# Kernel tuning notes

Measured on AMD Instinct MI355X. Metric: run time of the kernel, lower is better.

## Reference

```python
import jax, jax.numpy as jnp
import numpy as np

B, S, HID, H = 1, 2048, 2048, 16
D = HID // H
EPS = 1e-6


def _rotate_half(x):
    x1, x2 = jnp.split(x, 2, axis=-1)
    return jnp.concatenate([-x2, x1], axis=-1)


def _apply_rope(q, k, cos, sin):
    # cos, sin: [S, D] -> broadcast over [B, H, S, D]
    c = cos[None, None, :, :]
    s = sin[None, None, :, :]
    return q * c + _rotate_half(q) * s, k * c + _rotate_half(k) * s


def _proj_heads(x, W):
    # x: [B,S,HID], W: [HID_out, HID_in] (torch Linear convention) -> [B,H,S,D]
    y = jnp.einsum('bsh,oh->bso', x, W)
    return y.reshape(B, S, H, D).transpose(0, 2, 1, 3)


def setup_inputs() -> dict:
    key = jax.random.key(0)
    ks = jax.random.split(key, 12)
    inp = {
        'hidden_states_mu': jax.random.normal(ks[0], (B, S, HID), jnp.float32),
        'hidden_states_log_sigma': jax.random.normal(ks[1], (B, S, HID), jnp.float32) * 0.1,
    }
    # proper rotary tables
    inv_freq = 1.0 / (10000.0 ** (np.arange(0, D, 2, dtype=np.float32) / D))
    pos = np.arange(S, dtype=np.float32)
    freqs = np.outer(pos, inv_freq)                      # [S, D/2]
    emb = np.concatenate([freqs, freqs], axis=-1)        # [S, D]
    inp['cos'] = jnp.asarray(np.cos(emb), jnp.float32)
    inp['sin'] = jnp.asarray(np.sin(emb), jnp.float32)
    names = ['Wq_mu', 'Wk_mu', 'Wv_mu', 'Wo_mu', 'Wq_sigma', 'Wk_sigma', 'Wv_sigma', 'Wo_sigma']
    for i, n in enumerate(names):
        inp[n] = jax.random.normal(ks[2 + i], (HID, HID), jnp.float32) * 0.02
    inp['tau'] = jnp.ones((1,), jnp.float32)
    return inp


def reference(hidden_states_mu, hidden_states_log_sigma, cos, sin,
              Wq_mu, Wk_mu, Wv_mu, Wo_mu,
              Wq_sigma, Wk_sigma, Wv_sigma, Wo_sigma, tau):
    q_mu = _proj_heads(hidden_states_mu, Wq_mu)
    k_mu = _proj_heads(hidden_states_mu, Wk_mu)
    v_mu = _proj_heads(hidden_states_mu, Wv_mu)
    q_ls = _proj_heads(hidden_states_log_sigma, Wq_sigma)
    k_ls = _proj_heads(hidden_states_log_sigma, Wk_sigma)
    v_ls = _proj_heads(hidden_states_log_sigma, Wv_sigma)

    q_mu, k_mu = _apply_rope(q_mu, k_mu, cos, sin)

    # squared W2 distance between means
    dot_mu = jnp.einsum('bhqd,bhkd->bhqk', q_mu, k_mu)
    dist_mu_sq = (jnp.sum(q_mu ** 2, -1)[..., :, None]
                  + jnp.sum(k_mu ** 2, -1)[..., None, :]
                  - 2.0 * dot_mu)

    # squared W2 distance between sigmas
    sig_q = jnp.exp(0.5 * q_ls)
    sig_k = jnp.exp(0.5 * k_ls)
    dot_s = jnp.einsum('bhqd,bhkd->bhqk', sig_q, sig_k)
    dist_sigma_sq = (jnp.sum(sig_q ** 2, -1)[..., :, None]
                     + jnp.sum(sig_k ** 2, -1)[..., None, :]
                     - 2.0 * dot_s)

    denom = jnp.abs(tau[0]) + EPS
    attn = jax.nn.softmax(-(dist_mu_sq + dist_sigma_sq) / denom, axis=-1)

    out_mu = jnp.einsum('bhqk,bhkd->bhqd', attn, v_mu)
    out_ls = jnp.einsum('bhqk,bhkd->bhqd', attn, v_ls)
    out_mu = out_mu.transpose(0, 2, 1, 3).reshape(B, S, HID)
    out_ls = out_ls.transpose(0, 2, 1, 3).reshape(B, S, HID)
    out_mu = jnp.einsum('bsh,oh->bso', out_mu, Wo_mu)
    out_ls = jnp.einsum('bsh,oh->bso', out_ls, Wo_sigma)
    return out_mu, out_ls
```

## Files before the change

kernel.cpp:

```cpp
#include <hip/hip_runtime.h>
#include <hip/hip_bf16.h>

#define S_LEN 2048
#define HIDDEN 2048
#define NH 16
#define HD 128

typedef short short8 __attribute__((ext_vector_type(8)));
typedef short short4_t __attribute__((ext_vector_type(4)));
typedef float floatx4 __attribute__((ext_vector_type(4)));

#define MS(x) ((size_t)(x) * (size_t)(1u << 20))
#define O_XMU_HI MS(0)
#define O_XLS_HI MS(4)
#define O_XMU_LO MS(8)
#define O_WQ_HI MS(12)
#define O_WK_HI MS(16)
#define O_WQ_LO MS(20)
#define O_WK_LO MS(24)
#define O_WV MS(28)
#define O_WQS MS(32)
#define O_WKS MS(36)
#define O_WVS MS(40)
#define O_WO MS(44)
#define O_WOS MS(48)
#define O_Y0F MS(52)
#define O_Y1F MS(60)
#define O_Y2 MS(68)
#define O_Y3 MS(72)
#define O_Y4 MS(76)
#define O_Y5 MS(80)
#define O_QCHI MS(84)
#define O_KCHI MS(92)
#define O_QCLO MS(100)
#define O_KCLO MS(104)
#define O_VT MS(0)
#define O_AOMU MS(8)
#define O_AOLS MS(12)
#define O_CK MS(16)

__device__ __forceinline__ short f2bf(float f) {
  __hip_bfloat16 h = __float2bfloat16(f);
  return __builtin_bit_cast(short, h);
}
__device__ __forceinline__ float bf2f(short s) {
  unsigned u = ((unsigned)(unsigned short)s) << 16;
  return __builtin_bit_cast(float, u);
}

typedef __attribute__((address_space(1))) const unsigned int guint;
typedef __attribute__((address_space(3))) unsigned int luint;
__device__ __forceinline__ void gll16(const void* g, void* l) {
  __builtin_amdgcn_global_load_lds((guint*)g, (luint*)l, 16, 0, 0);
}

__global__ __launch_bounds__(256) void cvt_all(
    const float* __restrict__ xmu, const float* __restrict__ xls,
    const float* __restrict__ wq, const float* __restrict__ wk,
    const float* __restrict__ wv, const float* __restrict__ wqs,
    const float* __restrict__ wks, const float* __restrict__ wvs,
    const float* __restrict__ wo, const float* __restrict__ wos,
    short* __restrict__ Sb) {
  const int z = blockIdx.z;
  const float* src;
  size_t ho;
  size_t lof = (size_t)-1;
  switch (z) {
    case 0: src = xmu; ho = O_XMU_HI; lof = O_XMU_LO; break;
    case 1: src = wq;  ho = O_WQ_HI;  lof = O_WQ_LO;  break;
    case 2: src = wk;  ho = O_WK_HI;  lof = O_WK_LO;  break;
    case 3: src = xls; ho = O_XLS_HI; break;
    case 4: src = wv;  ho = O_WV;  break;
    case 5: src = wqs; ho = O_WQS; break;
    case 6: src = wks; ho = O_WKS; break;
    case 7: src = wvs; ho = O_WVS; break;
    case 8: src = wo;  ho = O_WO;  break;
    default: src = wos; ho = O_WOS; break;
  }
  const size_t i = ((size_t)blockIdx.x * 256 + threadIdx.x) * 4;
  const float4 v = *(const float4*)(src + i);
  short4_t h, l;
  h.x = f2bf(v.x); h.y = f2bf(v.y); h.z = f2bf(v.z); h.w = f2bf(v.w);
  *(short4_t*)(Sb + ho + i) = h;
  if (lof != (size_t)-1) {
    l.x = f2bf(v.x - bf2f(h.x));
    l.y = f2bf(v.y - bf2f(h.y));
    l.z = f2bf(v.z - bf2f(h.z));
    l.w = f2bf(v.w - bf2f(h.w));
    *(short4_t*)(Sb + lof + i) = l;
  }
}

__global__ __launch_bounds__(256) void gemm_all(short* __restrict__ Sb) {
  __shared__ __attribute__((aligned(16))) short As[128 * 32];
  __shared__ __attribute__((aligned(16))) short Bs[128 * 32];
  __shared__ __attribute__((aligned(16))) short Asl[128 * 32];
  __shared__ __attribute__((aligned(16))) short Bsl[128 * 32];
  const int z = blockIdx.z;
  const bool x3 = (z < 2);
  const short* A = Sb + ((z < 3) ? O_XMU_HI : O_XLS_HI);
  const size_t bo = (z == 0) ? O_WQ_HI : (z == 1) ? O_WK_HI : (z == 2) ? O_WV
                   : (z == 3) ? O_WQS : (z == 4) ? O_WKS : O_WVS;
  const short* B = Sb + bo;
  const short* ALo = Sb + O_XMU_LO;
  const short* BLo = Sb + ((z == 0) ? O_WQ_LO : O_WK_LO);
  float* Cf = (float*)(Sb + ((z == 0) ? O_Y0F : O_Y1F));
  short* Cb = Sb + O_Y2 + (size_t)(x3 ? 0 : (z - 2)) * MS(4);

  const int m0 = blockIdx.y * 128, n0 = blockIdx.x * 128;
  const int tid = threadIdx.x, lane = tid & 63, wave = tid >> 6;
  const int wr = wave >> 1, wc = wave & 1;
  const int lr = lane >> 2;
  const int lc = (lane & 3) * 8;
  const int fr = lane & 15, koff = (lane >> 4) * 8;

  floatx4 acc[4][4];
#pragma unroll
  for (int i = 0; i < 4; ++i)
#pragma unroll
    for (int j = 0; j < 4; ++j) acc[i][j] = 0.0f;

  for (int k0 = 0; k0 < HIDDEN; k0 += 32) {
#pragma unroll
    for (int j = 0; j < 2; ++j) {
      const int chunk = j * 4 + wave;
      gll16(A + (size_t)(m0 + chunk * 16 + lr) * HIDDEN + k0 + lc, &As[chunk * 512]);
      gll16(B + (size_t)(n0 + chunk * 16 + lr) * HIDDEN + k0 + lc, &Bs[chunk * 512]);
      if (x3) {
        gll16(ALo + (size_t)(m0 + chunk * 16 + lr) * HIDDEN + k0 + lc, &Asl[chunk * 512]);
        gll16(BLo + (size_t)(n0 + chunk * 16 + lr) * HIDDEN + k0 + lc, &Bsl[chunk * 512]);
      }
    }
    __syncthreads();
    short8 af[4], bf[4], afl[4], bfl[4];
#pragma unroll
    for (int i = 0; i < 4; ++i) {
      af[i] = *(const short8*)&As[(wr * 64 + i * 16 + fr) * 32 + koff];
      if (x3) afl[i] = *(const short8*)&Asl[(wr * 64 + i * 16 + fr) * 32 + koff];
    }
#pragma unroll
    for (int j = 0; j < 4; ++j) {
      bf[j] = *(const short8*)&Bs[(wc * 64 + j * 16 + fr) * 32 + koff];
      if (x3) bfl[j] = *(const short8*)&Bsl[(wc * 64 + j * 16 + fr) * 32 + koff];
    }
#pragma unroll
    for (int i = 0; i < 4; ++i)
#pragma unroll
      for (int j = 0; j < 4; ++j) {
        acc[i][j] = __builtin_amdgcn_mfma_f32_16x16x32_bf16(af[i], bf[j], acc[i][j], 0, 0, 0);
        if (x3) {
          acc[i][j] = __builtin_amdgcn_mfma_f32_16x16x32_bf16(af[i], bfl[j], acc[i][j], 0, 0, 0);
          acc[i][j] = __builtin_amdgcn_mfma_f32_16x16x32_bf16(afl[i], bf[j], acc[i][j], 0, 0, 0);
        }
      }
    __syncthreads();
  }

  const int cr = (lane >> 4) * 4, cc = lane & 15;
#pragma unroll
  for (int i = 0; i < 4; ++i)
#pragma unroll
    for (int j = 0; j < 4; ++j) {
      const int rowb = m0 + wr * 64 + i * 16 + cr;
      const int col = n0 + wc * 64 + j * 16 + cc;
#pragma unroll
      for (int r = 0; r < 4; ++r) {
        const float v = acc[i][j][r];
        if (x3) {
          Cf[(size_t)(rowb + r) * HIDDEN + col] = v;
        } else {
          Cb[(size_t)(rowb + r) * HIDDEN + col] = f2bf(v);
        }
      }
    }
}

__global__ __launch_bounds__(256) void gemm_plain(
    const short* __restrict__ Ah, int lda, longlong4 aoff,
    const short* __restrict__ Bh, int ldb, long long strideB,
    int K,
    float* __restrict__ C, int ldc, long long strideC) {
  __shared__ __attribute__((aligned(16))) short As[128 * 32];
  __shared__ __attribute__((aligned(16))) short Bs[128 * 32];
  const int z = blockIdx.z;
  const long long ao = (z == 0) ? aoff.x : (z == 1) ? aoff.y : (z == 2) ? aoff.z : aoff.w;
  const short* A = Ah + ao;
  const short* B = Bh + (long long)z * strideB;
  const int m0 = blockIdx.y * 128, n0 = blockIdx.x * 128;
  const int tid = threadIdx.x, lane = tid & 63, wave = tid >> 6;
  const int wr = wave >> 1, wc = wave & 1;
  const int lr = lane >> 2;
  const int lc = (lane & 3) * 8;
  const int fr = lane & 15, koff = (lane >> 4) * 8;

  floatx4 acc[4][4];
#pragma unroll
  for (int i = 0; i < 4; ++i)
#pragma unroll
    for (int j = 0; j < 4; ++j) acc[i][j] = 0.0f;

  for (int k0 = 0; k0 < K; k0 += 32) {
#pragma unroll
    for (int j = 0; j < 2; ++j) {
      const int chunk = j * 4 + wave;
      gll16(A + (size_t)(m0 + chunk * 16 + lr) * lda + k0 + lc, &As[chunk * 512]);
      gll16(B + (size_t)(n0 + chunk * 16 + lr) * ldb + k0 + lc, &Bs[chunk * 512]);
    }
    __syncthreads();
    short8 af[4], bf[4];
#pragma unroll
    for (int i = 0; i < 4; ++i)
      af[i] = *(const short8*)&As[(wr * 64 + i * 16 + fr) * 32 + koff];
#pragma unroll
    for (int j = 0; j < 4; ++j)
      bf[j] = *(const short8*)&Bs[(wc * 64 + j * 16 + fr) * 32 + koff];
#pragma unroll
    for (int i = 0; i < 4; ++i)
#pragma unroll
      for (int j = 0; j < 4; ++j)
        acc[i][j] = __builtin_amdgcn_mfma_f32_16x16x32_bf16(af[i], bf[j], acc[i][j], 0, 0, 0);
    __syncthreads();
  }

  const int cr = (lane >> 4) * 4, cc = lane & 15;
#pragma unroll
  for (int i = 0; i < 4; ++i)
#pragma unroll
    for (int j = 0; j < 4; ++j) {
      const int rowb = m0 + wr * 64 + i * 16 + cr;
      const int col = n0 + wc * 64 + j * 16 + cc;
#pragma unroll
      for (int r = 0; r < 4; ++r)
        C[(long long)z * strideC + (size_t)(rowb + r) * ldc + col] = acc[i][j][r];
    }
}

__global__ __launch_bounds__(128) void build_qk(
    const float* __restrict__ Yq, const float* __restrict__ Yk,
    const short* __restrict__ Yqs, const short* __restrict__ Yks,
    const float* __restrict__ cosp, const float* __restrict__ sinp,
    short* __restrict__ QChi, short* __restrict__ QClo,
    short* __restrict__ KChi, short* __restrict__ KClo, float* __restrict__ ck) {
  const int s = blockIdx.x;
  const int h = blockIdx.y;
  const int d = threadIdx.x;
  const size_t base = (size_t)s * HIDDEN + h * HD;
  const float c = cosp[s * HD + d];
  const float sn = sinp[s * HD + d];
  const float q = Yq[base + d];
  const float qp = Yq[base + (d ^ 64)];
  const float k = Yk[base + d];
  const float kp = Yk[base + (d ^ 64)];
  const float qr = q * c + ((d < 64) ? -qp : qp) * sn;
  const float kr = k * c + ((d < 64) ? -kp : kp) * sn;
  const float aq = expm1f(0.5f * bf2f(Yqs[base + d]));
  const float ak = expm1f(0.5f * bf2f(Yks[base + d]));
  const size_t grp = (size_t)h * 128 + (s >> 4);
  const int s16 = s & 15;
  const size_t o_hi_d = grp * 4096 + (d >> 3) * 128 + s16 * 8 + (d & 7);
  const size_t o_hi_a = grp * 4096 + ((128 + d) >> 3) * 128 + s16 * 8 + (d & 7);
  const size_t o_lo_d = grp * 2048 + (d >> 3) * 128 + s16 * 8 + (d & 7);
  const short qh = f2bf(qr), kh = f2bf(kr);
  QChi[o_hi_d] = qh;
  QClo[o_lo_d] = f2bf(qr - bf2f(qh));
  QChi[o_hi_a] = f2bf(aq);
  KChi[o_hi_d] = kh;
  KClo[o_lo_d] = f2bf(kr - bf2f(kh));
  KChi[o_hi_a] = f2bf(ak);

  float val = kr * kr + ak * ak;
#pragma unroll
  for (int off = 32; off > 0; off >>= 1) val += __shfl_down(val, off);
  __shared__ float red[2];
  if ((d & 63) == 0) red[d >> 6] = val;
  __syncthreads();
  if (d == 0) ck[(size_t)h * S_LEN + s] = red[0] + red[1];
}

__global__ __launch_bounds__(256) void build_vt(const short* __restrict__ Yv,
                                                const short* __restrict__ Yvs,
                                                short* __restrict__ VT) {
  __shared__ short tile[32][33];
  const int s0 = blockIdx.x * 32;
  const int n0 = blockIdx.y * 32;
  const int h = blockIdx.z;
  const int tid = threadIdx.x;
  const int tx = tid & 31;
  const int ty = tid >> 5;
  const short* src = (n0 < HD) ? Yv : Yvs;
  const int c0 = n0 & (HD - 1);
#pragma unroll
  for (int r = ty; r < 32; r += 8)
    tile[r][tx] = src[(size_t)(s0 + r) * HIDDEN + h * HD + c0 + tx];
  __syncthreads();
  if (tid < 128) {
    const int nl = tid >> 2;
    const int s8 = tid & 3;
    short8 v;
#pragma unroll
    for (int e = 0; e < 8; ++e) v[e] = tile[s8 * 8 + e][nl];
    const int n = n0 + nl;
    const int kv8 = (s0 >> 3) + s8;
    const size_t off = (size_t)h * 524288 + (size_t)(n >> 4) * 32768 + (size_t)kv8 * 128 +
                       (n & 15) * 8;
    *(short8*)&VT[off] = v;
  }
}

__global__ __launch_bounds__(256, 2) void fa_kernel(
    const short* __restrict__ QChi, const short* __restrict__ QClo,
    const short* __restrict__ KChi, const short* __restrict__ KClo,
    const short* __restrict__ VT, const float* __restrict__ ck,
    const float* __restrict__ tau,
    short* __restrict__ AOmu, short* __restrict__ AOls) {
  __shared__ __attribute__((aligned(16))) short kchi[2][8192];
  __shared__ __attribute__((aligned(16))) short vt[2][8192];
  __shared__ __attribute__((aligned(16))) short patch[2048];

  const int bid = blockIdx.x + 32 * blockIdx.y;
  const int wg = ((bid & 7) << 6) + (bid >> 3);
  const int qt = wg & 31;
  const int h = wg >> 5;
  const int tid = threadIdx.x;
  const int lane = tid & 63;
  const int w = tid >> 6;
  const int qgrp = qt * 4 + w;
  const float inv = 1.0f / (fabsf(tau[0]) + 1e-6f);

  const short* QChi_h = QChi + (size_t)h * 524288;
  const short* QClo_h = QClo + (size_t)h * 262144;
  const short* KChi_h = KChi + (size_t)h * 524288;
  const short* KClo_h = KClo + (size_t)h * 262144;
  const short* VT_h = VT + (size_t)h * 524288;
  const float* ckh = ck + (size_t)h * S_LEN;

  short8 qhi[8], qlo[4];
#pragma unroll
  for (int ks = 0; ks < 8; ++ks)
    qhi[ks] = *(const short8*)&QChi_h[(size_t)qgrp * 4096 + ks * 512 + lane * 8];
#pragma unroll
  for (int ks = 0; ks < 4; ++ks)
    qlo[ks] = *(const short8*)&QClo_h[(size_t)qgrp * 2048 + ks * 512 + lane * 8];

  floatx4 o[16];
#pragma unroll
  for (int nf = 0; nf < 16; ++nf) o[nf] = 0.0f;
  float m_[4], l_[4];
#pragma unroll
  for (int r = 0; r < 4; ++r) { m_[r] = -1e30f; l_[r] = 0.0f; }

  short* patchw = &patch[w * 512];

#pragma unroll
  for (int i = 0; i < 4; ++i) {
    const int c = w * 4 + i;
    gll16(KChi_h + (size_t)(c >> 3) * 4096 + (c & 7) * 512 + lane * 8,
          &kchi[0][c * 512]);
  }
#pragma unroll
  for (int i = 0; i < 4; ++i) {
    const int c = w * 4 + i;
    gll16(VT_h + (size_t)c * 32768 + lane * 8, &vt[0][c * 512]);
  }

  for (int t = 0; t < 64; ++t) {
    const int cur = t & 1;
    asm volatile("s_waitcnt vmcnt(0)" ::: "memory");
    __builtin_amdgcn_s_barrier();

    short8 klo[8];
#pragma unroll
    for (int j = 0; j < 8; ++j)
      klo[j] = *(const short8*)&KClo_h[(size_t)(2 * t + (j >> 2)) * 2048 +
                                       (j & 3) * 512 + lane * 8];

    if (t < 63) {
#pragma unroll
      for (int i = 0; i < 4; ++i) {
        const int c = w * 4 + i;
        gll16(KChi_h + (size_t)(2 * (t + 1) + (c >> 3)) * 4096 + (c & 7) * 512 + lane * 8,
              &kchi[cur ^ 1][c * 512]);
      }
#pragma unroll
      for (int i = 0; i < 4; ++i) {
        const int c = w * 4 + i;
        gll16(VT_h + (size_t)c * 32768 + (t + 1) * 512 + lane * 8,
              &vt[cur ^ 1][c * 512]);
      }
    }

    __builtin_amdgcn_s_setprio(1);
    floatx4 s0 = 0.0f, s1 = 0.0f;
    short8 h0[4], h1[4];
#pragma unroll
    for (int ks = 0; ks < 8; ++ks) {
      const short8 b0 = *(const short8*)&kchi[cur][ks * 512 + lane * 8];
      const short8 b1 = *(const short8*)&kchi[cur][(8 + ks) * 512 + lane * 8];
      s0 = __builtin_amdgcn_mfma_f32_16x16x32_bf16(qhi[ks], b0, s0, 0, 0, 0);
      s1 = __builtin_amdgcn_mfma_f32_16x16x32_bf16(qhi[ks], b1, s1, 0, 0, 0);
      if (ks < 4) { h0[ks] = b0; h1[ks] = b1; }
    }
#pragma unroll
    for (int ks = 0; ks < 4; ++ks) {
      s0 = __builtin_amdgcn_mfma_f32_16x16x32_bf16(qhi[ks], klo[ks], s0, 0, 0, 0);
      s1 = __builtin_amdgcn_mfma_f32_16x16x32_bf16(qhi[ks], klo[4 + ks], s1, 0, 0, 0);
      s0 = __builtin_amdgcn_mfma_f32_16x16x32_bf16(qlo[ks], h0[ks], s0, 0, 0, 0);
      s1 = __builtin_amdgcn_mfma_f32_16x16x32_bf16(qlo[ks], h1[ks], s1, 0, 0, 0);
    }
    __builtin_amdgcn_s_setprio(0);

    const float ck0 = ckh[t * 32 + (lane & 15)];
    const float ck1 = ckh[t * 32 + 16 + (lane & 15)];
    float L0[4], L1[4], p0[4], p1[4];
    bool okl = true;
#pragma unroll
    for (int r = 0; r < 4; ++r) {
      L0[r] = (2.0f * s0[r] - ck0) * inv;
      L1[r] = (2.0f * s1[r] - ck1) * inv;
      okl = okl && (fmaxf(L0[r], L1[r]) <= m_[r] + 8.0f);
    }
    if (__all(okl)) {
#pragma unroll
      for (int r = 0; r < 4; ++r) {
        p0[r] = __expf(L0[r] - m_[r]);
        p1[r] = __expf(L1[r] - m_[r]);
        l_[r] += p0[r] + p1[r];
      }
    } else {
#pragma unroll
      for (int r = 0; r < 4; ++r) {
        float mx = fmaxf(L0[r], L1[r]);
        mx = fmaxf(mx, __shfl_xor(mx, 1));
        mx = fmaxf(mx, __shfl_xor(mx, 2));
        mx = fmaxf(mx, __shfl_xor(mx, 4));
        mx = fmaxf(mx, __shfl_xor(mx, 8));
        const float mnew = fmaxf(m_[r], mx);
        const float alpha = __expf(m_[r] - mnew);
        m_[r] = mnew;
        p0[r] = __expf(L0[r] - mnew);
        p1[r] = __expf(L1[r] - mnew);
        l_[r] = l_[r] * alpha + p0[r] + p1[r];
#pragma unroll
        for (int nf = 0; nf < 16; ++nf) o[nf][r] *= alpha;
      }
    }

    {
      const int row = (lane >> 4) * 4;
      const int c0i = lane & 15;
      const int c1i = 16 + (lane & 15);
#pragma unroll
      for (int r = 0; r < 4; ++r) {
        patchw[(c0i >> 3) * 128 + (row + r) * 8 + (c0i & 7)] = f2bf(p0[r]);
        patchw[(c1i >> 3) * 128 + (row + r) * 8 + (c1i & 7)] = f2bf(p1[r]);
      }
    }
    asm volatile("s_waitcnt lgkmcnt(0)\n" ::: "memory");
    const short8 pa = *(const short8*)&patchw[lane * 8];

    __builtin_amdgcn_s_setprio(1);
#pragma unroll
    for (int nf = 0; nf < 16; ++nf) {
      const short8 vf = *(const short8*)&vt[cur][nf * 512 + lane * 8];
      o[nf] = __builtin_amdgcn_mfma_f32_16x16x32_bf16(pa, vf, o[nf], 0, 0, 0);
    }
    __builtin_amdgcn_s_setprio(0);
  }

  float rs[4];
#pragma unroll
  for (int r = 0; r < 4; ++r) {
    float lv = l_[r];
    lv += __shfl_xor(lv, 1);
    lv += __shfl_xor(lv, 2);
    lv += __shfl_xor(lv, 4);
    lv += __shfl_xor(lv, 8);
    rs[r] = 1.0f / lv;
  }
  const int qbase = qgrp * 16 + (lane >> 4) * 4;
#pragma unroll
  for (int nf = 0; nf < 16; ++nf) {
    const int n = nf * 16 + (lane & 15);
    short* dst = (n < HD) ? AOmu : AOls;
    const int col = h * HD + (n & (HD - 1));
#pragma unroll
    for (int r = 0; r < 4; ++r)
      dst[(size_t)(qbase + r) * HIDDEN + col] = f2bf(o[nf][r] * rs[r]);
  }
}

extern "C" void kernel_launch(void* const* d_in, const int* in_sizes, int n_in,
                              void* d_out, int out_size, void* d_ws, size_t ws_size,
                              hipStream_t stream) {
  (void)in_sizes; (void)n_in; (void)out_size; (void)ws_size;
  const float* Xmu = (const float*)d_in[0];
  const float* Xls = (const float*)d_in[1];
  const float* cosp = (const float*)d_in[2];
  const float* sinp = (const float*)d_in[3];
  const float* Wq_mu = (const float*)d_in[4];
  const float* Wk_mu = (const float*)d_in[5];
  const float* Wv_mu = (const float*)d_in[6];
  const float* Wo_mu = (const float*)d_in[7];
  const float* Wq_s = (const float*)d_in[8];
  const float* Wk_s = (const float*)d_in[9];
  const float* Wv_s = (const float*)d_in[10];
  const float* Wo_s = (const float*)d_in[11];
  const float* tau = (const float*)d_in[12];

  float* out = (float*)d_out;
  short* S = (short*)d_ws;
  const long long M4 = (long long)MS(4);

  cvt_all<<<dim3(4096, 1, 10), 256, 0, stream>>>(Xmu, Xls, Wq_mu, Wk_mu, Wv_mu, Wq_s,
                                                 Wk_s, Wv_s, Wo_mu, Wo_s, S);

  gemm_all<<<dim3(16, 16, 6), 256, 0, stream>>>(S);

  build_qk<<<dim3(S_LEN, NH), 128, 0, stream>>>(
      (const float*)(S + O_Y0F), (const float*)(S + O_Y1F), S + O_Y3, S + O_Y4,
      cosp, sinp, S + O_QCHI, S + O_QCLO, S + O_KCHI, S + O_KCLO,
      (float*)(S + O_CK));
  build_vt<<<dim3(S_LEN / 32, 256 / 32, NH), 256, 0, stream>>>(S + O_Y2, S + O_Y5,
                                                               S + O_VT);

  fa_kernel<<<dim3(32, NH), 256, 0, stream>>>(
      S + O_QCHI, S + O_QCLO, S + O_KCHI, S + O_KCLO, S + O_VT,
      (const float*)(S + O_CK), tau, S + O_AOMU, S + O_AOLS);

  {
    longlong4 ao = {0, (long long)MS(4), 0, 0};
    gemm_plain<<<dim3(16, 16, 2), 256, 0, stream>>>(
        S + O_AOMU, HIDDEN, ao, S + O_WO, HIDDEN, M4, HIDDEN,
        out, HIDDEN, 4194304);
  }
}
```

Baseline: 646.5 us.

## Split-K output projection and single-buffer V tile for higher attention occupancy

The output projection GEMM is split into two K-halves across 4 z-slices, giving 1024 blocks instead of 512, and a new combine kernel sums the partials. The attention kernel drops the V double buffer and loads each V tile at the start of its iteration, with an extra barrier before the PV MFMAs. This cuts LDS so launch bounds can request 3 blocks per SM. The costs are exposed V load latency, an extra barrier per iteration, and an extra pass over 64MB of fp32 partials.

```diff
diff --git a/kernel.cpp b/kernel.cpp
--- a/kernel.cpp
+++ b/kernel.cpp
@@ -38,6 +38,7 @@
 #define O_AOMU MS(8)
 #define O_AOLS MS(12)
 #define O_CK MS(16)
+#define O_PK MS(52)
 
 __device__ __forceinline__ short f2bf(float f) {
   __hip_bfloat16 h = __float2bfloat16(f);
@@ -175,17 +176,15 @@
     }
 }
 
-__global__ __launch_bounds__(256) void gemm_plain(
-    const short* __restrict__ Ah, int lda, longlong4 aoff,
-    const short* __restrict__ Bh, int ldb, long long strideB,
-    int K,
-    float* __restrict__ C, int ldc, long long strideC) {
+__global__ __launch_bounds__(256) void gemm_out(const short* __restrict__ Sb,
+                                                float* __restrict__ PK) {
   __shared__ __attribute__((aligned(16))) short As[128 * 32];
   __shared__ __attribute__((aligned(16))) short Bs[128 * 32];
-  const int z = blockIdx.z;
-  const long long ao = (z == 0) ? aoff.x : (z == 1) ? aoff.y : (z == 2) ? aoff.z : aoff.w;
-  const short* A = Ah + ao;
-  const short* B = Bh + (long long)z * strideB;
+  const int zz = blockIdx.z;
+  const int proj = zz >> 1, kh = zz & 1;
+  const short* A = Sb + (proj ? O_AOLS : O_AOMU) + kh * 1024;
+  const short* B = Sb + (proj ? O_WOS : O_WO) + kh * 1024;
+  float* C = PK + (size_t)zz * 4194304;
   const int m0 = blockIdx.y * 128, n0 = blockIdx.x * 128;
   const int tid = threadIdx.x, lane = tid & 63, wave = tid >> 6;
   const int wr = wave >> 1, wc = wave & 1;
@@ -199,12 +198,12 @@
 #pragma unroll
     for (int j = 0; j < 4; ++j) acc[i][j] = 0.0f;
 
-  for (int k0 = 0; k0 < K; k0 += 32) {
+  for (int k0 = 0; k0 < 1024; k0 += 32) {
 #pragma unroll
     for (int j = 0; j < 2; ++j) {
       const int chunk = j * 4 + wave;
-      gll16(A + (size_t)(m0 + chunk * 16 + lr) * lda + k0 + lc, &As[chunk * 512]);
-      gll16(B + (size_t)(n0 + chunk * 16 + lr) * ldb + k0 + lc, &Bs[chunk * 512]);
+      gll16(A + (size_t)(m0 + chunk * 16 + lr) * HIDDEN + k0 + lc, &As[chunk * 512]);
+      gll16(B + (size_t)(n0 + chunk * 16 + lr) * HIDDEN + k0 + lc, &Bs[chunk * 512]);
     }
     __syncthreads();
     short8 af[4], bf[4];
@@ -231,8 +230,19 @@
       const int col = n0 + wc * 64 + j * 16 + cc;
 #pragma unroll
       for (int r = 0; r < 4; ++r)
-        C[(long long)z * strideC + (size_t)(rowb + r) * ldc + col] = acc[i][j][r];
-    }
+        C[(size_t)(rowb + r) * HIDDEN + col] = acc[i][j][r];
+    }
+}
+
+__global__ __launch_bounds__(256) void combine_out(const float* __restrict__ PK,
+                                                   float* __restrict__ out) {
+  const size_t i = ((size_t)blockIdx.x * 256 + threadIdx.x) * 4;
+  const size_t po = (size_t)blockIdx.y * 8388608;
+  const float4 a = *(const float4*)(PK + po + i);
+  const float4 b = *(const float4*)(PK + po + 4194304 + i);
+  float4 r;
+  r.x = a.x + b.x; r.y = a.y + b.y; r.z = a.z + b.z; r.w = a.w + b.w;
+  *(float4*)(out + (size_t)blockIdx.y * 4194304 + i) = r;
 }
 
 __global__ __launch_bounds__(128) void build_qk(
@@ -307,14 +317,14 @@
   }
 }
 
-__global__ __launch_bounds__(256, 2) void fa_kernel(
+__global__ __launch_bounds__(256, 3) void fa_kernel(
     const short* __restrict__ QChi, const short* __restrict__ QClo,
     const short* __restrict__ KChi, const short* __restrict__ KClo,
     const short* __restrict__ VT, const float* __restrict__ ck,
     const float* __restrict__ tau,
     short* __restrict__ AOmu, short* __restrict__ AOls) {
   __shared__ __attribute__((aligned(16))) short kchi[2][8192];
-  __shared__ __attribute__((aligned(16))) short vt[2][8192];
+  __shared__ __attribute__((aligned(16))) short vt[8192];
   __shared__ __attribute__((aligned(16))) short patch[2048];
 
   const int bid = blockIdx.x + 32 * blockIdx.y;
@@ -357,17 +367,18 @@
     gll16(KChi_h + (size_t)(c >> 3) * 4096 + (c & 7) * 512 + lane * 8,
           &kchi[0][c * 512]);
   }
-#pragma unroll
-  for (int i = 0; i < 4; ++i) {
-    const int c = w * 4 + i;
-    gll16(VT_h + (size_t)c * 32768 + lane * 8, &vt[0][c * 512]);
-  }
 
   for (int t = 0; t < 64; ++t) {
     const int cur = t & 1;
     asm volatile("s_waitcnt vmcnt(0)" ::: "memory");
     __builtin_amdgcn_s_barrier();
 
+#pragma unroll
+    for (int i = 0; i < 4; ++i) {
+      const int c = w * 4 + i;
+      gll16(VT_h + (size_t)c * 32768 + t * 512 + lane * 8, &vt[c * 512]);
+    }
+
     short8 klo[8];
 #pragma unroll
     for (int j = 0; j < 8; ++j)
@@ -380,12 +391,6 @@
         const int c = w * 4 + i;
         gll16(KChi_h + (size_t)(2 * (t + 1) + (c >> 3)) * 4096 + (c & 7) * 512 + lane * 8,
               &kchi[cur ^ 1][c * 512]);
-      }
-#pragma unroll
-      for (int i = 0; i < 4; ++i) {
-        const int c = w * 4 + i;
-        gll16(VT_h + (size_t)c * 32768 + (t + 1) * 512 + lane * 8,
-              &vt[cur ^ 1][c * 512]);
       }
     }
 
@@ -458,10 +463,12 @@
     asm volatile("s_waitcnt lgkmcnt(0)\n" ::: "memory");
     const short8 pa = *(const short8*)&patchw[lane * 8];
 
+    __builtin_amdgcn_s_barrier();
+
     __builtin_amdgcn_s_setprio(1);
 #pragma unroll
     for (int nf = 0; nf < 16; ++nf) {
-      const short8 vf = *(const short8*)&vt[cur][nf * 512 + lane * 8];
+      const short8 vf = *(const short8*)&vt[nf * 512 + lane * 8];
       o[nf] = __builtin_amdgcn_mfma_f32_16x16x32_bf16(pa, vf, o[nf], 0, 0, 0);
     }
     __builtin_amdgcn_s_setprio(0);
@@ -509,7 +516,6 @@
 
   float* out = (float*)d_out;
   short* S = (short*)d_ws;
-  const long long M4 = (long long)MS(4);
 
   cvt_all<<<dim3(4096, 1, 10), 256, 0, stream>>>(Xmu, Xls, Wq_mu, Wk_mu, Wv_mu, Wq_s,
                                                  Wk_s, Wv_s, Wo_mu, Wo_s, S);
@@ -527,10 +533,6 @@
       S + O_QCHI, S + O_QCLO, S + O_KCHI, S + O_KCLO, S + O_VT,
       (const float*)(S + O_CK), tau, S + O_AOMU, S + O_AOLS);
 
-  {
-    longlong4 ao = {0, (long long)MS(4), 0, 0};
-    gemm_plain<<<dim3(16, 16, 2), 256, 0, stream>>>(
-        S + O_AOMU, HIDDEN, ao, S + O_WO, HIDDEN, M4, HIDDEN,
-        out, HIDDEN, 4194304);
-  }
-}
+  gemm_out<<<dim3(16, 16, 4), 256, 0, stream>>>(S, (float*)(S + O_PK));
+  combine_out<<<dim3(4096, 2), 256, 0, stream>>>((const float*)(S + O_PK), out);
+}
```

Result: slower. 1.080 ms (+67.1%).
